# Kernel optimization log

Measured on AMD Instinct MI355X. Metric: run time of the kernel, lower is better.

Reference implementation:

```python
import jax, jax.numpy as jnp
import numpy as np

B = 64
N_TEXT, N_VIS, N_AC = 256, 32, 32
N = N_TEXT + N_VIS + N_AC  # 320 total graph nodes
HID, HEADS, LAYERS = 512, 8, 2
HEAD_DIM = HID // HEADS
SW_K, SW_P, SF_M, ALPHA, CROSS_P = 6, 0.15, 3, 0.5, 0.3


def build_hybrid_adj():
    """Watts-Strogatz + Barabasi-Albert hybrid adjacency with cross-modal edges (numpy, setup only)."""
    rng = np.random.default_rng(0)
    # small-world ring lattice
    sw = np.zeros((N, N), np.float32)
    idx = np.arange(N)
    for j in range(1, SW_K // 2 + 1):
        sw[idx, (idx + j) % N] = 1.0
        sw[idx, (idx - j) % N] = 1.0
    # rewiring
    for i in range(N):
        for j in range(i + 1, N):
            if sw[i, j] == 1 and rng.random() < SW_P:
                sw[i, j] = sw[j, i] = 0.0
                cand = np.where(sw[i] == 0)[0]
                cand = cand[cand != i]
                if len(cand) > 0:
                    nj = rng.choice(cand)
                    sw[i, nj] = sw[nj, i] = 1.0
    # scale-free (Barabasi-Albert)
    sf = np.zeros((N, N), np.float32)
    for i in range(SF_M + 1):
        for j in range(i + 1, SF_M + 1):
            sf[i, j] = sf[j, i] = 1.0
    deg = sf.sum(1)
    for v in range(SF_M + 1, N):
        prob = deg[:v] / deg[:v].sum()
        targets = rng.choice(v, size=min(SF_M, v), replace=False, p=prob)
        sf[v, targets] = 1.0
        sf[targets, v] = 1.0
        deg = sf.sum(1)
    adj = ((ALPHA * sw + (1.0 - ALPHA) * sf) > 0.3).astype(np.float32)
    # cross-modal edges: text<->visual, text<->acoustic (Bernoulli), visual<->acoustic temporal diagonal
    ts, te = 0, N_TEXT
    vs, ve = te, te + N_VIS
    as_, ae = ve, ve + N_AC
    cm_v = (rng.random((N_TEXT, N_VIS)) < CROSS_P).astype(np.float32)
    adj[ts:te, vs:ve] = np.maximum(adj[ts:te, vs:ve], cm_v)
    adj[vs:ve, ts:te] = adj[ts:te, vs:ve].T
    cm_a = (rng.random((N_TEXT, N_AC)) < CROSS_P).astype(np.float32)
    adj[ts:te, as_:ae] = np.maximum(adj[ts:te, as_:ae], cm_a)
    adj[as_:ae, ts:te] = adj[ts:te, as_:ae].T
    k = min(N_VIS, N_AC)
    adj[vs + np.arange(k), as_ + np.arange(k)] = 1.0
    adj[as_ + np.arange(k), vs + np.arange(k)] = 1.0
    return adj.astype(np.int32)


def setup_inputs() -> dict:
    key = jax.random.key(0)
    ks = jax.random.split(key, 12)
    s = 0.02
    return {
        "text": jax.random.normal(ks[0], (B, N_TEXT, 768), jnp.float32),
        "visual": jax.random.normal(ks[1], (B, N_VIS, 47), jnp.float32),
        "acoustic": jax.random.normal(ks[2], (B, N_AC, 74), jnp.float32),
        "adj": jnp.asarray(build_hybrid_adj()),
        "Wt": jax.random.normal(ks[3], (768, HID), jnp.float32) * s,
        "Wv": jax.random.normal(ks[4], (47, HID), jnp.float32) * s,
        "Wa": jax.random.normal(ks[5], (74, HID), jnp.float32) * s,
        "Wg": jax.random.normal(ks[6], (LAYERS, HEADS, HID, HEAD_DIM), jnp.float32) * s,
        "a_src": jax.random.normal(ks[7], (LAYERS, HEADS, HEAD_DIM), jnp.float32) * s,
        "a_dst": jax.random.normal(ks[8], (LAYERS, HEADS, HEAD_DIM), jnp.float32) * s,
        "edge_logits": jax.random.normal(ks[9], (N, N), jnp.float32) * s,
    }


def _fusion(text, visual, acoustic, adj, Wt, Wv, Wa, Wg, a_src, a_dst, edge_logits):
    # project each modality into shared hidden space and stack as graph nodes
    x = jnp.concatenate([
        jnp.einsum("btd,dh->bth", text, Wt),
        jnp.einsum("bvd,dh->bvh", visual, Wv),
        jnp.einsum("bad,dh->bah", acoustic, Wa),
    ], axis=1)  # [B, N, HID]
    mask = (adj != 0)[None, None, :, :]  # [1,1,N,N]
    for l in range(LAYERS):
        h = jnp.einsum("bnd,hdf->bhnf", x, Wg[l])          # [B,H,N,Fh]
        # a([h_i || h_j]) factorizes: e_ij = a_src.h_i + a_dst.h_j
        fi = jnp.einsum("bhnf,hf->bhn", h, a_src[l])
        fj = jnp.einsum("bhnf,hf->bhn", h, a_dst[l])
        e = jax.nn.leaky_relu(fi[:, :, :, None] + fj[:, :, None, :], 0.2)
        e = e + edge_logits[None, None, :, :]               # learnable topology bias
        e = jnp.where(mask, e, -jnp.inf)                    # adjacency-masked scores
        att = jnp.nan_to_num(jax.nn.softmax(e, axis=-1))    # fully-masked rows -> 0
        out = jnp.einsum("bhij,bhjf->bhif", att, h)         # message passing
        x = out.transpose(0, 2, 1, 3).reshape(x.shape[0], N, HID)  # concat heads
        if l < LAYERS - 1:
            x = jax.nn.elu(x)
    return x  # [B, N, HID] fused node embeddings


def reference(text, visual, acoustic, adj, Wt, Wv, Wa, Wg, a_src, a_dst, edge_logits):
    return _fusion(text, visual, acoustic, adj, Wt, Wv, Wa, Wg, a_src, a_dst, edge_logits)
```

## Files before the change

### kernel.cpp

```cpp
#include <hip/hip_runtime.h>
#include <hip/hip_bf16.h>
#include <math.h>

#define BB 64
#define NN 320
#define NT 256
#define NV 32
#define NA 32
#define HIDD 512
#define NHEAD 8
#define FD 64

#define LDK 40

typedef __attribute__((ext_vector_type(8))) short bf16x8;
typedef __attribute__((ext_vector_type(4))) float floatx4;

__device__ float me_g[NN * NN];
__device__ float fif_g[512 * NN];
__device__ float fjf_g[512 * NN];

__device__ __forceinline__ void split1(float v, unsigned short& h, unsigned short& l) {
    unsigned u = __float_as_uint(v);
    unsigned hu = u & 0xFFFF0000u;
    float lf = v - __uint_as_float(hu);
    h = (unsigned short)(hu >> 16);
    l = (unsigned short)(__float_as_uint(lf) >> 16);
}
__device__ __forceinline__ unsigned pack2(unsigned short a, unsigned short b) {
    return (unsigned)a | ((unsigned)b << 16);
}

__global__ __launch_bounds__(256) void build_me(
    const int* __restrict__ adj, const float* __restrict__ elog)
{
    const int i4 = (blockIdx.x * 256 + threadIdx.x) * 4;
    const int4   a = *(const int4*)&adj[i4];
    const float4 e = *(const float4*)&elog[i4];
    float4 m;
    m.x = a.x ? __expf(e.x) : 0.f;
    m.y = a.y ? __expf(e.y) : 0.f;
    m.z = a.z ? __expf(e.z) : 0.f;
    m.w = a.w ? __expf(e.w) : 0.f;
    *(float4*)&me_g[i4] = m;
}

__global__ __launch_bounds__(256) void gemm_mfma(
    const float* __restrict__ A, const float* __restrict__ Bsrc,
    float* __restrict__ C, unsigned short* __restrict__ Hthi,
    unsigned short* __restrict__ Htlo, const float* __restrict__ asrc,
    const float* __restrict__ adst, int M, int K, int b_mode, int rpb, int noff)
{
    __shared__ unsigned short Ah[128 * LDK];
    __shared__ unsigned short Al[128 * LDK];
    __shared__ unsigned short Bh[128 * LDK];
    __shared__ unsigned short Bl[128 * LDK];

    const int tid  = threadIdx.x;
    const int lane = tid & 63;
    const int w    = tid >> 6;
    const int rw   = w >> 1, cw = w & 1;
    const int m0   = blockIdx.x * 128;
    const int n0   = blockIdx.y * 128;

    floatx4 acc[4][4];
#pragma unroll
    for (int s = 0; s < 4; s++)
#pragma unroll
        for (int t = 0; t < 4; t++) acc[s][t] = (floatx4)0.f;

    const int arow = tid >> 1;
    const int akh  = (tid & 1) * 16;
    const int bc   = tid & 127;
    const int bkh  = (tid >> 7) * 16;
    const int bhead = (n0 + bc) >> 6;
    const int bf    = (n0 + bc) & 63;

    const int afrag0 = (rw * 64 + (lane & 15)) * LDK + (lane >> 4) * 8;
    const int bfrag0 = (cw * 64 + (lane & 15)) * LDK + (lane >> 4) * 8;

    for (int k0 = 0; k0 < K; k0 += 32) {
        __syncthreads();
        {
            const float* ga = A + (size_t)(m0 + arow) * K + k0 + akh;
            const int la = arow * LDK + akh;
            if (k0 + 32 <= K) {
#pragma unroll
                for (int u = 0; u < 4; u++) {
                    float4 v = *(const float4*)(ga + 4 * u);
                    unsigned short h0,h1,h2,h3,l0,l1,l2,l3;
                    split1(v.x,h0,l0); split1(v.y,h1,l1);
                    split1(v.z,h2,l2); split1(v.w,h3,l3);
                    *(uint2*)&Ah[la + 4*u] = make_uint2(pack2(h0,h1), pack2(h2,h3));
                    *(uint2*)&Al[la + 4*u] = make_uint2(pack2(l0,l1), pack2(l2,l3));
                }
            } else {
#pragma unroll
                for (int u = 0; u < 16; u++) {
                    float v = (k0 + akh + u < K) ? ga[u] : 0.f;
                    unsigned short h, l; split1(v, h, l);
                    Ah[la + u] = h; Al[la + u] = l;
                }
            }
        }
        {
            unsigned short hb[16], lb[16];
#pragma unroll
            for (int u = 0; u < 16; u++) {
                int k = k0 + bkh + u;
                float v;
                if (k < K) {
                    size_t gi = b_mode
                        ? (size_t)bhead * (512 * 64) + (size_t)k * 64 + bf
                        : (size_t)k * 512 + n0 + bc;
                    v = Bsrc[gi];
                } else v = 0.f;
                split1(v, hb[u], lb[u]);
            }
            const int lb0 = bc * LDK + bkh;
#pragma unroll
            for (int u = 0; u < 4; u++) {
                *(uint2*)&Bh[lb0 + 4*u] = make_uint2(pack2(hb[4*u],hb[4*u+1]), pack2(hb[4*u+2],hb[4*u+3]));
                *(uint2*)&Bl[lb0 + 4*u] = make_uint2(pack2(lb[4*u],lb[4*u+1]), pack2(lb[4*u+2],lb[4*u+3]));
            }
        }
        __syncthreads();

        bf16x8 ah[4], al[4], bh[4], bl[4];
#pragma unroll
        for (int s = 0; s < 4; s++) {
            ah[s] = *(const bf16x8*)&Ah[afrag0 + s * 16 * LDK];
            al[s] = *(const bf16x8*)&Al[afrag0 + s * 16 * LDK];
        }
#pragma unroll
        for (int t = 0; t < 4; t++) {
            bh[t] = *(const bf16x8*)&Bh[bfrag0 + t * 16 * LDK];
            bl[t] = *(const bf16x8*)&Bl[bfrag0 + t * 16 * LDK];
        }
#pragma unroll
        for (int s = 0; s < 4; s++)
#pragma unroll
            for (int t = 0; t < 4; t++) {
                acc[s][t] = __builtin_amdgcn_mfma_f32_16x16x32_bf16(ah[s], bh[t], acc[s][t], 0, 0, 0);
                acc[s][t] = __builtin_amdgcn_mfma_f32_16x16x32_bf16(ah[s], bl[t], acc[s][t], 0, 0, 0);
                acc[s][t] = __builtin_amdgcn_mfma_f32_16x16x32_bf16(al[s], bh[t], acc[s][t], 0, 0, 0);
            }
    }

    if (b_mode == 0) {
#pragma unroll
        for (int s = 0; s < 4; s++) {
            const int gr0 = m0 + rw * 64 + s * 16 + (lane >> 4) * 4;
#pragma unroll
            for (int r = 0; r < 4; r++) {
                const unsigned grow = gr0 + r;
                const unsigned b = grow / (unsigned)rpb;
                const unsigned rr = grow - b * rpb;
                float* crow = C + ((size_t)b * NN + noff + rr) * HIDD;
#pragma unroll
                for (int t = 0; t < 4; t++) {
                    crow[n0 + cw * 64 + t * 16 + (lane & 15)] = acc[s][t][r];
                }
            }
        }
    } else {
        const int hd = (n0 + cw * 64) >> 6;
        const int fq = lane & 15;
#pragma unroll
        for (int s = 0; s < 4; s++) {
            const int m_s = m0 + rw * 64 + s * 16 + (lane >> 4) * 4;
            const unsigned b = (unsigned)m_s / 320u;
            const int jb = m_s - b * 320;
            const int ks = jb >> 5;
            const int jg2 = (jb >> 3) & 3;
            const int eb = jb & 7;
            const size_t slab = (size_t)b * 8 + hd;
#pragma unroll
            for (int t = 0; t < 4; t++) {
                unsigned short h0,h1,h2,h3,l0,l1,l2,l3;
                split1(acc[s][t][0],h0,l0); split1(acc[s][t][1],h1,l1);
                split1(acc[s][t][2],h2,l2); split1(acc[s][t][3],h3,l3);
                const size_t base = (((slab * 10 + ks) * 4 + t) * 512
                                     + (size_t)(fq | (jg2 << 4)) * 8) + eb;
                *(uint2*)&Hthi[base] = make_uint2(pack2(h0,h1), pack2(h2,h3));
                *(uint2*)&Htlo[base] = make_uint2(pack2(l0,l1), pack2(l2,l3));
            }
        }
        float as4[4], ad4[4];
#pragma unroll
        for (int t = 0; t < 4; t++) {
            as4[t] = asrc[hd * 64 + t * 16 + fq];
            ad4[t] = adst[hd * 64 + t * 16 + fq];
        }
#pragma unroll
        for (int s = 0; s < 4; s++) {
            const int m_s = m0 + rw * 64 + s * 16 + (lane >> 4) * 4;
            const unsigned b = (unsigned)m_s / 320u;
            const int jb = m_s - b * 320;
            float4 fi4, fj4;
#pragma unroll
            for (int r = 0; r < 4; r++) {
                float fi = (acc[s][0][r]*as4[0] + acc[s][1][r]*as4[1])
                         + (acc[s][2][r]*as4[2] + acc[s][3][r]*as4[3]);
                float fj = (acc[s][0][r]*ad4[0] + acc[s][1][r]*ad4[1])
                         + (acc[s][2][r]*ad4[2] + acc[s][3][r]*ad4[3]);
#pragma unroll
                for (int d = 1; d < 16; d <<= 1) {
                    fi += __shfl_xor(fi, d);
                    fj += __shfl_xor(fj, d);
                }
                ((float*)&fi4)[r] = fi; ((float*)&fj4)[r] = fj;
            }
            if (fq == 0) {
                const size_t o = ((size_t)b * 8 + hd) * NN + jb;
                *(float4*)&fif_g[o] = fi4;
                *(float4*)&fjf_g[o] = fj4;
            }
        }
    }
}

template<int IP0, int NIP>
__device__ __forceinline__ void attn_body(
    const unsigned short* __restrict__ Hthi, const unsigned short* __restrict__ Htlo,
    float* __restrict__ xout, int apply_elu, float* fjs, float* ls)
{
    const int bh = blockIdx.x;
    const int hd = bh & 7, b = bh >> 3;
    const int tid = threadIdx.x, lane = tid & 63, w = tid >> 6;
    const int fq = lane & 15, jg = lane >> 4;

    for (int r = tid; r < NN; r += 256) fjs[r] = fjf_g[bh * NN + r];

    float fir[NIP];
#pragma unroll
    for (int ip = 0; ip < NIP; ip++)
        fir[ip] = fif_g[bh * NN + (IP0 + ip) * 64 + (w << 4) + fq];
    __syncthreads();

    floatx4 acc[NIP][4];
#pragma unroll
    for (int ip = 0; ip < NIP; ip++)
#pragma unroll
        for (int nt = 0; nt < 4; nt++) acc[ip][nt] = (floatx4)0.f;
    float lacc[NIP];
#pragma unroll
    for (int ip = 0; ip < NIP; ip++) lacc[ip] = 0.f;

    for (int ks = 0; ks < 10; ks++) {
        const int j8 = ks * 32 + jg * 8;
        const float4 fj0 = *(const float4*)&fjs[j8];
        const float4 fj1 = *(const float4*)&fjs[j8 + 4];

        bf16x8 ahh[NIP], all[NIP];
#pragma unroll
        for (int ip = 0; ip < NIP; ip++) {
            const int i = (IP0 + ip) * 64 + (w << 4) + fq;
            const float fiv = fir[ip];
            const unsigned g = (unsigned)i * NN + j8;
            const float4 m0 = *(const float4*)&me_g[g];
            const float4 m1 = *(const float4*)&me_g[g + 4];
            float p[8];
            {
                float s;
                s = fiv + fj0.x; s = fmaxf(s, 0.2f*s); p[0] = __expf(s) * m0.x;
                s = fiv + fj0.y; s = fmaxf(s, 0.2f*s); p[1] = __expf(s) * m0.y;
                s = fiv + fj0.z; s = fmaxf(s, 0.2f*s); p[2] = __expf(s) * m0.z;
                s = fiv + fj0.w; s = fmaxf(s, 0.2f*s); p[3] = __expf(s) * m0.w;
                s = fiv + fj1.x; s = fmaxf(s, 0.2f*s); p[4] = __expf(s) * m1.x;
                s = fiv + fj1.y; s = fmaxf(s, 0.2f*s); p[5] = __expf(s) * m1.y;
                s = fiv + fj1.z; s = fmaxf(s, 0.2f*s); p[6] = __expf(s) * m1.z;
                s = fiv + fj1.w; s = fmaxf(s, 0.2f*s); p[7] = __expf(s) * m1.w;
            }
            lacc[ip] += ((p[0]+p[1]) + (p[2]+p[3])) + ((p[4]+p[5]) + (p[6]+p[7]));

            unsigned short ph[8], pl[8];
#pragma unroll
            for (int e = 0; e < 8; e++) split1(p[e], ph[e], pl[e]);
            union { uint4 u; bf16x8 v; } ua, ul;
            ua.u = make_uint4(pack2(ph[0],ph[1]), pack2(ph[2],ph[3]),
                              pack2(ph[4],ph[5]), pack2(ph[6],ph[7]));
            ul.u = make_uint4(pack2(pl[0],pl[1]), pack2(pl[2],pl[3]),
                              pack2(pl[4],pl[5]), pack2(pl[6],pl[7]));
            ahh[ip] = ua.v; all[ip] = ul.v;
        }

#pragma unroll
        for (int nt = 0; nt < 4; nt++) {
            const unsigned off = (((unsigned)bh * 10 + ks) * 4 + nt) * 512 + (unsigned)lane * 8;
            const bf16x8 bhf = *(const bf16x8*)&Hthi[off];
            const bf16x8 blf = *(const bf16x8*)&Htlo[off];
#pragma unroll
            for (int ip = 0; ip < NIP; ip++) {
                acc[ip][nt] = __builtin_amdgcn_mfma_f32_16x16x32_bf16(ahh[ip], bhf, acc[ip][nt], 0, 0, 0);
                acc[ip][nt] = __builtin_amdgcn_mfma_f32_16x16x32_bf16(ahh[ip], blf, acc[ip][nt], 0, 0, 0);
                acc[ip][nt] = __builtin_amdgcn_mfma_f32_16x16x32_bf16(all[ip], bhf, acc[ip][nt], 0, 0, 0);
            }
        }
    }

#pragma unroll
    for (int ip = 0; ip < NIP; ip++) {
        float l = lacc[ip];
        l += __shfl_xor(l, 16);
        l += __shfl_xor(l, 32);
        if (jg == 0) ls[(IP0 + ip) * 64 + (w << 4) + fq] = l;
    }
    __syncthreads();

#pragma unroll
    for (int ip = 0; ip < NIP; ip++) {
        const int ib = ((IP0 + ip) * 4 + w) * 16 + jg * 4;
#pragma unroll
        for (int r = 0; r < 4; r++) {
            const float lv = ls[ib + r];
            const float inv = (lv > 0.f) ? 1.f / lv : 0.f;
            float* orow = xout + ((size_t)(b * NN + ib + r)) * HIDD + hd * 64;
#pragma unroll
            for (int nt = 0; nt < 4; nt++) {
                float vv = acc[ip][nt][r] * inv;
                if (apply_elu) vv = (vv > 0.f) ? vv : __expf(vv) - 1.f;
                orow[nt * 16 + fq] = vv;
            }
        }
    }
}

__global__ __launch_bounds__(256, 4) void attn_mfma(
    const unsigned short* __restrict__ Hthi, const unsigned short* __restrict__ Htlo,
    float* __restrict__ xout, int apply_elu)
{
    __shared__ float fjs[NN];
    __shared__ float ls[NN];
    if (blockIdx.y == 0) attn_body<0, 3>(Hthi, Htlo, xout, apply_elu, fjs, ls);
    else                 attn_body<3, 2>(Hthi, Htlo, xout, apply_elu, fjs, ls);
}

extern "C" void kernel_launch(void* const* d_in, const int* in_sizes, int n_in,
                              void* d_out, int out_size, void* d_ws, size_t ws_size,
                              hipStream_t stream)
{
    (void)in_sizes; (void)n_in; (void)out_size; (void)ws_size;
    const float* text     = (const float*)d_in[0];
    const float* visual   = (const float*)d_in[1];
    const float* acoustic = (const float*)d_in[2];
    const int*   adj      = (const int*)d_in[3];
    const float* Wt       = (const float*)d_in[4];
    const float* Wv       = (const float*)d_in[5];
    const float* Wa       = (const float*)d_in[6];
    const float* Wg       = (const float*)d_in[7];
    const float* a_src    = (const float*)d_in[8];
    const float* a_dst    = (const float*)d_in[9];
    const float* elog     = (const float*)d_in[10];

    float* xbuf = (float*)d_out;
    unsigned short* Hthi = (unsigned short*)d_ws;
    unsigned short* Htlo = Hthi + (size_t)512 * 10 * 4 * 512;

    build_me<<<NN * NN / 1024, 256, 0, stream>>>(adj, elog);

    gemm_mfma<<<dim3((BB*NT)/128, 4), 256, 0, stream>>>(text,     Wt, xbuf, nullptr, nullptr, nullptr, nullptr, BB*NT, 768, 0, NT, 0);
    gemm_mfma<<<dim3((BB*NV)/128, 4), 256, 0, stream>>>(visual,   Wv, xbuf, nullptr, nullptr, nullptr, nullptr, BB*NV,  47, 0, NV, NT);
    gemm_mfma<<<dim3((BB*NA)/128, 4), 256, 0, stream>>>(acoustic, Wa, xbuf, nullptr, nullptr, nullptr, nullptr, BB*NA,  74, 0, NA, NT + NV);

    for (int l = 0; l < 2; l++) {
        const float* Wg_l = Wg + (size_t)l * NHEAD * HIDD * FD;
        gemm_mfma<<<dim3((BB*NN)/128, 4), 256, 0, stream>>>(xbuf, Wg_l, nullptr, Hthi, Htlo,
            a_src + l * NHEAD * FD, a_dst + l * NHEAD * FD, BB*NN, HIDD, 1, NN, 0);
        attn_mfma<<<dim3(BB * NHEAD, 2), 256, 0, stream>>>(
            Hthi, Htlo, xbuf, (l == 0) ? 1 : 0);
    }
}
```

Measured before the change: 372.1 us.

## Pre-split operands into bf16 hi/lo global buffers and load MFMA fragments directly

Operands are converted to bf16 hi/lo pairs once, in separate presplit kernels for the inputs and weights. Weights are stored in MFMA-fragment order, and the previous layer's epilogue writes split activations. The GEMM then drops its LDS staging and barriers and reads fragments straight from global memory into registers. This removes the repeated per-tile split work and LDS traffic, at the cost of extra launches, extra global writes of split copies, and uncoalesced, unshared global fragment loads with no prefetch.

Result: slower. 458.8 us (+23.3%).

```diff
diff --git a/kernel.cpp b/kernel.cpp
--- a/kernel.cpp
+++ b/kernel.cpp
@@ -11,14 +11,22 @@
 #define NHEAD 8
 #define FD 64
 
-#define LDK 40
-
 typedef __attribute__((ext_vector_type(8))) short bf16x8;
 typedef __attribute__((ext_vector_type(4))) float floatx4;
 
 __device__ float me_g[NN * NN];
 __device__ float fif_g[512 * NN];
 __device__ float fjf_g[512 * NN];
+__device__ unsigned short tihi_g[16384 * 768];
+__device__ unsigned short tilo_g[16384 * 768];
+__device__ unsigned short vihi_g[2048 * 64];
+__device__ unsigned short vilo_g[2048 * 64];
+__device__ unsigned short achi_g[2048 * 128];
+__device__ unsigned short aclo_g[2048 * 128];
+__device__ unsigned short xhi_g[20480 * 512];
+__device__ unsigned short xlo_g[20480 * 512];
+__device__ unsigned short bwhi_g[512 * 768];
+__device__ unsigned short bwlo_g[512 * 768];
 
 __device__ __forceinline__ void split1(float v, unsigned short& h, unsigned short& l) {
     unsigned u = __float_as_uint(v);
@@ -45,23 +53,67 @@
     *(float4*)&me_g[i4] = m;
 }
 
-__global__ __launch_bounds__(256) void gemm_mfma(
-    const float* __restrict__ A, const float* __restrict__ Bsrc,
-    float* __restrict__ C, unsigned short* __restrict__ Hthi,
-    unsigned short* __restrict__ Htlo, const float* __restrict__ asrc,
-    const float* __restrict__ adst, int M, int K, int b_mode, int rpb, int noff)
-{
-    __shared__ unsigned short Ah[128 * LDK];
-    __shared__ unsigned short Al[128 * LDK];
-    __shared__ unsigned short Bh[128 * LDK];
-    __shared__ unsigned short Bl[128 * LDK];
-
-    const int tid  = threadIdx.x;
-    const int lane = tid & 63;
-    const int w    = tid >> 6;
-    const int rw   = w >> 1, cw = w & 1;
-    const int m0   = blockIdx.x * 128;
-    const int n0   = blockIdx.y * 128;
+__global__ __launch_bounds__(256) void presplit_A(
+    const float* __restrict__ src, int M, int K, int Kp, int sel)
+{
+    unsigned short* dh = (sel == 0) ? tihi_g : (sel == 1) ? vihi_g : achi_g;
+    unsigned short* dl = (sel == 0) ? tilo_g : (sel == 1) ? vilo_g : aclo_g;
+    const long long i4 = ((long long)blockIdx.x * 256 + threadIdx.x) * 4;
+    if (i4 >= (long long)M * Kp) return;
+    const int row = (int)(i4 / Kp);
+    const int k = (int)(i4 - (long long)row * Kp);
+    float v[4];
+    if (((K & 3) == 0) && (k + 4 <= K)) {
+        const float4 f = *(const float4*)&src[(size_t)row * K + k];
+        v[0] = f.x; v[1] = f.y; v[2] = f.z; v[3] = f.w;
+    } else {
+#pragma unroll
+        for (int e = 0; e < 4; e++) v[e] = (k + e < K) ? src[(size_t)row * K + k + e] : 0.f;
+    }
+    unsigned short h[4], l[4];
+#pragma unroll
+    for (int e = 0; e < 4; e++) split1(v[e], h[e], l[e]);
+    *(uint2*)&dh[i4] = make_uint2(pack2(h[0], h[1]), pack2(h[2], h[3]));
+    *(uint2*)&dl[i4] = make_uint2(pack2(l[0], l[1]), pack2(l[2], l[3]));
+}
+
+__global__ __launch_bounds__(64) void presplit_B(
+    const float* __restrict__ W, int K, int Kp, int wg_mode)
+{
+    const int lane = threadIdx.x;
+    const int nt = blockIdx.x, kt = blockIdx.y;
+    const int col = nt * 16 + (lane & 15);
+    const int k0 = kt * 32 + (lane >> 4) * 8;
+    unsigned short h[8], l[8];
+#pragma unroll
+    for (int e = 0; e < 8; e++) {
+        const int k = k0 + e;
+        float v = 0.f;
+        if (k < K) v = wg_mode ? W[(size_t)(col >> 6) * (512 * 64) + (size_t)k * 64 + (col & 63)]
+                               : W[(size_t)k * 512 + col];
+        split1(v, h[e], l[e]);
+    }
+    const size_t o = (((size_t)nt * (Kp >> 5) + kt) * 64 + lane) * 8;
+    *(uint4*)&bwhi_g[o] = make_uint4(pack2(h[0], h[1]), pack2(h[2], h[3]),
+                                     pack2(h[4], h[5]), pack2(h[6], h[7]));
+    *(uint4*)&bwlo_g[o] = make_uint4(pack2(l[0], l[1]), pack2(l[2], l[3]),
+                                     pack2(l[4], l[5]), pack2(l[6], l[7]));
+}
+
+__global__ __launch_bounds__(256, 3) void gemm_reg(
+    unsigned short* __restrict__ Hthi, unsigned short* __restrict__ Htlo,
+    const float* __restrict__ asrc, const float* __restrict__ adst,
+    int Kp, int a_sel, int b_mode, int rpb, int noff)
+{
+    const unsigned short* Ahi = (a_sel == 0) ? tihi_g : (a_sel == 1) ? vihi_g
+                              : (a_sel == 2) ? achi_g : xhi_g;
+    const unsigned short* Alo = (a_sel == 0) ? tilo_g : (a_sel == 1) ? vilo_g
+                              : (a_sel == 2) ? aclo_g : xlo_g;
+
+    const int tid = threadIdx.x, lane = tid & 63, w = tid >> 6;
+    const int rw = w >> 1, cw = w & 1;
+    const int m0 = blockIdx.x * 128, n0 = blockIdx.y * 128;
+    const int nk = Kp >> 5;
 
     floatx4 acc[4][4];
 #pragma unroll
@@ -69,85 +121,36 @@
 #pragma unroll
         for (int t = 0; t < 4; t++) acc[s][t] = (floatx4)0.f;
 
-    const int arow = tid >> 1;
-    const int akh  = (tid & 1) * 16;
-    const int bc   = tid & 127;
-    const int bkh  = (tid >> 7) * 16;
-    const int bhead = (n0 + bc) >> 6;
-    const int bf    = (n0 + bc) & 63;
-
-    const int afrag0 = (rw * 64 + (lane & 15)) * LDK + (lane >> 4) * 8;
-    const int bfrag0 = (cw * 64 + (lane & 15)) * LDK + (lane >> 4) * 8;
-
-    for (int k0 = 0; k0 < K; k0 += 32) {
-        __syncthreads();
-        {
-            const float* ga = A + (size_t)(m0 + arow) * K + k0 + akh;
-            const int la = arow * LDK + akh;
-            if (k0 + 32 <= K) {
-#pragma unroll
-                for (int u = 0; u < 4; u++) {
-                    float4 v = *(const float4*)(ga + 4 * u);
-                    unsigned short h0,h1,h2,h3,l0,l1,l2,l3;
-                    split1(v.x,h0,l0); split1(v.y,h1,l1);
-                    split1(v.z,h2,l2); split1(v.w,h3,l3);
-                    *(uint2*)&Ah[la + 4*u] = make_uint2(pack2(h0,h1), pack2(h2,h3));
-                    *(uint2*)&Al[la + 4*u] = make_uint2(pack2(l0,l1), pack2(l2,l3));
-                }
-            } else {
-#pragma unroll
-                for (int u = 0; u < 16; u++) {
-                    float v = (k0 + akh + u < K) ? ga[u] : 0.f;
-                    unsigned short h, l; split1(v, h, l);
-                    Ah[la + u] = h; Al[la + u] = l;
-                }
-            }
-        }
-        {
-            unsigned short hb[16], lb[16];
-#pragma unroll
-            for (int u = 0; u < 16; u++) {
-                int k = k0 + bkh + u;
-                float v;
-                if (k < K) {
-                    size_t gi = b_mode
-                        ? (size_t)bhead * (512 * 64) + (size_t)k * 64 + bf
-                        : (size_t)k * 512 + n0 + bc;
-                    v = Bsrc[gi];
-                } else v = 0.f;
-                split1(v, hb[u], lb[u]);
-            }
-            const int lb0 = bc * LDK + bkh;
-#pragma unroll
-            for (int u = 0; u < 4; u++) {
-                *(uint2*)&Bh[lb0 + 4*u] = make_uint2(pack2(hb[4*u],hb[4*u+1]), pack2(hb[4*u+2],hb[4*u+3]));
-                *(uint2*)&Bl[lb0 + 4*u] = make_uint2(pack2(lb[4*u],lb[4*u+1]), pack2(lb[4*u+2],lb[4*u+3]));
-            }
-        }
-        __syncthreads();
-
-        bf16x8 ah[4], al[4], bh[4], bl[4];
+    const unsigned abase = (unsigned)(m0 + rw * 64 + (lane & 15)) * Kp + ((lane >> 4) << 3);
+    const unsigned tgb = blockIdx.y * 8 + cw * 4;
+    const unsigned bbase = (tgb * (unsigned)nk * 64 + lane) * 8;
+
+    for (int kt = 0; kt < nk; kt++) {
+        bf16x8 a_h[4], a_l[4], b_h[4], b_l[4];
 #pragma unroll
         for (int s = 0; s < 4; s++) {
-            ah[s] = *(const bf16x8*)&Ah[afrag0 + s * 16 * LDK];
-            al[s] = *(const bf16x8*)&Al[afrag0 + s * 16 * LDK];
+            const unsigned ao = abase + (unsigned)s * 16 * Kp + (unsigned)kt * 32;
+            a_h[s] = *(const bf16x8*)&Ahi[ao];
+            a_l[s] = *(const bf16x8*)&Alo[ao];
         }
 #pragma unroll
         for (int t = 0; t < 4; t++) {
-            bh[t] = *(const bf16x8*)&Bh[bfrag0 + t * 16 * LDK];
-            bl[t] = *(const bf16x8*)&Bl[bfrag0 + t * 16 * LDK];
+            const unsigned bo = bbase + ((unsigned)t * nk + kt) * 512;
+            b_h[t] = *(const bf16x8*)&bwhi_g[bo];
+            b_l[t] = *(const bf16x8*)&bwlo_g[bo];
         }
 #pragma unroll
         for (int s = 0; s < 4; s++)
 #pragma unroll
             for (int t = 0; t < 4; t++) {
-                acc[s][t] = __builtin_amdgcn_mfma_f32_16x16x32_bf16(ah[s], bh[t], acc[s][t], 0, 0, 0);
-                acc[s][t] = __builtin_amdgcn_mfma_f32_16x16x32_bf16(ah[s], bl[t], acc[s][t], 0, 0, 0);
-                acc[s][t] = __builtin_amdgcn_mfma_f32_16x16x32_bf16(al[s], bh[t], acc[s][t], 0, 0, 0);
+                acc[s][t] = __builtin_amdgcn_mfma_f32_16x16x32_bf16(a_h[s], b_h[t], acc[s][t], 0, 0, 0);
+                acc[s][t] = __builtin_amdgcn_mfma_f32_16x16x32_bf16(a_h[s], b_l[t], acc[s][t], 0, 0, 0);
+                acc[s][t] = __builtin_amdgcn_mfma_f32_16x16x32_bf16(a_l[s], b_h[t], acc[s][t], 0, 0, 0);
             }
     }
 
     if (b_mode == 0) {
+        const int fq = lane & 15;
 #pragma unroll
         for (int s = 0; s < 4; s++) {
             const int gr0 = m0 + rw * 64 + s * 16 + (lane >> 4) * 4;
@@ -156,10 +159,12 @@
                 const unsigned grow = gr0 + r;
                 const unsigned b = grow / (unsigned)rpb;
                 const unsigned rr = grow - b * rpb;
-                float* crow = C + ((size_t)b * NN + noff + rr) * HIDD;
+                const size_t ro = ((size_t)b * NN + noff + rr) * HIDD + n0 + cw * 64 + fq;
 #pragma unroll
                 for (int t = 0; t < 4; t++) {
-                    crow[n0 + cw * 64 + t * 16 + (lane & 15)] = acc[s][t][r];
+                    unsigned short h, l; split1(acc[s][t][r], h, l);
+                    xhi_g[ro + t * 16] = h;
+                    xlo_g[ro + t * 16] = l;
                 }
             }
         }
@@ -223,7 +228,7 @@
 template<int IP0, int NIP>
 __device__ __forceinline__ void attn_body(
     const unsigned short* __restrict__ Hthi, const unsigned short* __restrict__ Htlo,
-    float* __restrict__ xout, int apply_elu, float* fjs, float* ls)
+    float* __restrict__ xout, int final_out, float* fjs, float* ls)
 {
     const int bh = blockIdx.x;
     const int hd = bh & 7, b = bh >> 3;
@@ -315,12 +320,20 @@
         for (int r = 0; r < 4; r++) {
             const float lv = ls[ib + r];
             const float inv = (lv > 0.f) ? 1.f / lv : 0.f;
-            float* orow = xout + ((size_t)(b * NN + ib + r)) * HIDD + hd * 64;
-#pragma unroll
-            for (int nt = 0; nt < 4; nt++) {
-                float vv = acc[ip][nt][r] * inv;
-                if (apply_elu) vv = (vv > 0.f) ? vv : __expf(vv) - 1.f;
-                orow[nt * 16 + fq] = vv;
+            const size_t ro = ((size_t)(b * NN + ib + r)) * HIDD + hd * 64;
+            if (final_out) {
+#pragma unroll
+                for (int nt = 0; nt < 4; nt++)
+                    xout[ro + nt * 16 + fq] = acc[ip][nt][r] * inv;
+            } else {
+#pragma unroll
+                for (int nt = 0; nt < 4; nt++) {
+                    float vv = acc[ip][nt][r] * inv;
+                    vv = (vv > 0.f) ? vv : __expf(vv) - 1.f;
+                    unsigned short h, l2; split1(vv, h, l2);
+                    xhi_g[ro + nt * 16 + fq] = h;
+                    xlo_g[ro + nt * 16 + fq] = l2;
+                }
             }
         }
     }
@@ -328,12 +341,12 @@
 
 __global__ __launch_bounds__(256, 4) void attn_mfma(
     const unsigned short* __restrict__ Hthi, const unsigned short* __restrict__ Htlo,
-    float* __restrict__ xout, int apply_elu)
+    float* __restrict__ xout, int final_out)
 {
     __shared__ float fjs[NN];
     __shared__ float ls[NN];
-    if (blockIdx.y == 0) attn_body<0, 3>(Hthi, Htlo, xout, apply_elu, fjs, ls);
-    else                 attn_body<3, 2>(Hthi, Htlo, xout, apply_elu, fjs, ls);
+    if (blockIdx.y == 0) attn_body<0, 3>(Hthi, Htlo, xout, final_out, fjs, ls);
+    else                 attn_body<3, 2>(Hthi, Htlo, xout, final_out, fjs, ls);
 }
 
 extern "C" void kernel_launch(void* const* d_in, const int* in_sizes, int n_in,
@@ -359,15 +372,26 @@
 
     build_me<<<NN * NN / 1024, 256, 0, stream>>>(adj, elog);
 
-    gemm_mfma<<<dim3((BB*NT)/128, 4), 256, 0, stream>>>(text,     Wt, xbuf, nullptr, nullptr, nullptr, nullptr, BB*NT, 768, 0, NT, 0);
-    gemm_mfma<<<dim3((BB*NV)/128, 4), 256, 0, stream>>>(visual,   Wv, xbuf, nullptr, nullptr, nullptr, nullptr, BB*NV,  47, 0, NV, NT);
-    gemm_mfma<<<dim3((BB*NA)/128, 4), 256, 0, stream>>>(acoustic, Wa, xbuf, nullptr, nullptr, nullptr, nullptr, BB*NA,  74, 0, NA, NT + NV);
+    presplit_A<<<(16384 * 768) / 1024, 256, 0, stream>>>(text,     16384, 768, 768, 0);
+    presplit_A<<<(2048 * 64)   / 1024, 256, 0, stream>>>(visual,   2048,  47,  64,  1);
+    presplit_A<<<(2048 * 128)  / 1024, 256, 0, stream>>>(acoustic, 2048,  74,  128, 2);
+
+    presplit_B<<<dim3(32, 768 / 32), 64, 0, stream>>>(Wt, 768, 768, 0);
+    gemm_reg<<<dim3((BB*NT)/128, 4), 256, 0, stream>>>(nullptr, nullptr, nullptr, nullptr,
+                                                       768, 0, 0, NT, 0);
+    presplit_B<<<dim3(32, 64 / 32), 64, 0, stream>>>(Wv, 47, 64, 0);
+    gemm_reg<<<dim3((BB*NV)/128, 4), 256, 0, stream>>>(nullptr, nullptr, nullptr, nullptr,
+                                                       64, 1, 0, NV, NT);
+    presplit_B<<<dim3(32, 128 / 32), 64, 0, stream>>>(Wa, 74, 128, 0);
+    gemm_reg<<<dim3((BB*NA)/128, 4), 256, 0, stream>>>(nullptr, nullptr, nullptr, nullptr,
+                                                       128, 2, 0, NA, NT + NV);
 
     for (int l = 0; l < 2; l++) {
         const float* Wg_l = Wg + (size_t)l * NHEAD * HIDD * FD;
-        gemm_mfma<<<dim3((BB*NN)/128, 4), 256, 0, stream>>>(xbuf, Wg_l, nullptr, Hthi, Htlo,
-            a_src + l * NHEAD * FD, a_dst + l * NHEAD * FD, BB*NN, HIDD, 1, NN, 0);
+        presplit_B<<<dim3(32, 512 / 32), 64, 0, stream>>>(Wg_l, 512, 512, 1);
+        gemm_reg<<<dim3((BB*NN)/128, 4), 256, 0, stream>>>(Hthi, Htlo,
+            a_src + l * NHEAD * FD, a_dst + l * NHEAD * FD, 512, 3, 1, NN, 0);
         attn_mfma<<<dim3(BB * NHEAD, 2), 256, 0, stream>>>(
-            Hthi, Htlo, xbuf, (l == 0) ? 1 : 0);
-    }
-}
+            Hthi, Htlo, xbuf, (l == 0) ? 0 : 1);
+    }
+}
```
